# Optimization experiments

Measured on AMD Instinct MI355X. Metric: run time of the kernel, lower is better.

Reference implementation:

```python
import jax, jax.numpy as jnp
import numpy as np

EPS_NORM = 1e-7   # Normalize module eps (added to norm)
EPS_COS = 1e-8    # torch F.cosine_similarity default eps (clamped denom)


def _normalize(x):
    # Normalize(power=2): x / (||x||_2 + 1e-7), norm over dim 1
    n = jnp.sqrt(jnp.sum(x * x, axis=1, keepdims=True))
    return x / (n + EPS_NORM)


def _cos_sim_matrix(f):
    # pairwise cosine similarity, matching torch cosine_similarity semantics:
    # (f_i . f_j) / max(||f_i|| * ||f_j||, eps)
    n = jnp.linalg.norm(f, axis=1)            # [N]
    denom = jnp.maximum(n[:, None] * n[None, :], EPS_COS)
    return (f @ f.T) / denom                   # [N, N]


def setup_inputs() -> dict:
    key = jax.random.key(0)
    kq, kk = jax.random.split(key)
    N, D = 4096, 1024
    feat_q = jax.random.normal(kq, (N, D), dtype=jnp.float32)
    feat_k = jax.random.normal(kk, (N, D), dtype=jnp.float32)
    return {"feat_q": feat_q, "feat_k": feat_k}


def reference(feat_q, feat_k):
    q = _normalize(feat_q)
    k = jax.lax.stop_gradient(_normalize(feat_k))  # feat_k.detach()
    Sq = _cos_sim_matrix(q)   # [N, N]
    Sk = _cos_sim_matrix(k)   # [N, N]
    N = feat_q.shape[0]
    off_diag = ~jnp.eye(N, dtype=bool)
    diff2 = (Sq - Sk) ** 2
    # mean over the N*(N-1) off-diagonal (i != j) pairs
    loss = jnp.sum(jnp.where(off_diag, diff2, 0.0)) / (N * (N - 1))
    return loss
```

## Files before the change

kernel.cpp:

```cpp
#include <hip/hip_runtime.h>
#include <hip/hip_bf16.h>
#include <stdint.h>

#define N_ROWS 4096
#define DIMS   1024
#define BM 128
#define BN 128
#define BK 64
#define TGRID 32
#define NTILES 528

typedef __attribute__((ext_vector_type(8))) short short8;
typedef __attribute__((ext_vector_type(4))) float f32x4;

__device__ __forceinline__ unsigned short f2bf(float f) {
  union { float f; unsigned int u; } c; c.f = f;
  unsigned int u = c.u;
  unsigned int r = (u + 0x7fffu + ((u >> 16) & 1u)) >> 16;
  return (unsigned short)r;
}

__device__ __forceinline__ void async_cp16(const unsigned short* g, void* lds) {
  __builtin_amdgcn_global_load_lds(
      (const __attribute__((address_space(1))) void*)g,
      (__attribute__((address_space(3))) void*)lds, 16, 0, 0);
}

__global__ __launch_bounds__(256) void normalize_bf16_kernel(
    const float* __restrict__ fq, const float* __restrict__ fk,
    unsigned short* __restrict__ qn, unsigned short* __restrict__ kn,
    float* __restrict__ out) {
  if (blockIdx.x == 0 && blockIdx.y == 0 && threadIdx.x == 0) out[0] = 0.0f;
  const int w = threadIdx.x >> 6;
  const int lane = threadIdx.x & 63;
  const int row = blockIdx.x * 4 + w;
  const float* src = blockIdx.y ? fk : fq;
  unsigned short* dst = blockIdx.y ? kn : qn;
  const float4* s4 = (const float4*)(src + (size_t)row * DIMS);
  float4 v[4];
  float ss = 0.0f;
  #pragma unroll
  for (int s = 0; s < 4; ++s) {
    v[s] = s4[lane + 64 * s];
    ss += v[s].x * v[s].x + v[s].y * v[s].y + v[s].z * v[s].z + v[s].w * v[s].w;
  }
  #pragma unroll
  for (int off = 32; off > 0; off >>= 1) ss += __shfl_xor(ss, off);
  const float scale = 1.0f / sqrtf(ss);
  ushort4* d4 = (ushort4*)(dst + (size_t)row * DIMS);
  #pragma unroll
  for (int s = 0; s < 4; ++s) {
    ushort4 o;
    o.x = f2bf(v[s].x * scale);
    o.y = f2bf(v[s].y * scale);
    o.z = f2bf(v[s].z * scale);
    o.w = f2bf(v[s].w * scale);
    d4[lane + 64 * s] = o;
  }
}

__global__ __launch_bounds__(256, 2) void constloss_main_kernel(
    const unsigned short* __restrict__ qn,
    const unsigned short* __restrict__ kn,
    float* __restrict__ out) {
  __shared__ __align__(16) char smem[4 * BM * BK * 2];

  int I = 0, rem = blockIdx.x;
  while (rem >= (TGRID - I)) { rem -= (TGRID - I); ++I; }
  const int J = I + rem;

  const int tid = threadIdx.x;
  const int w = tid >> 6;
  const int lane = tid & 63;

  const unsigned short* sbase = (w & 2) ? kn : qn;
  const int rblk = (w & 1) ? J : I;
  const unsigned short* srow = sbase + (size_t)rblk * BM * DIMS;
  const int rl = lane >> 3;
  const int cl = (lane & 7) ^ rl;
  const unsigned short* gsrc0 = srow + (size_t)rl * DIMS + cl * 8;
  char* ldsTile = smem + w * (BM * BK * 2);

  const int wr = w >> 1, wc = w & 1;
  const int ml = lane & 15;
  const int quad = lane >> 4;
  const int ar0 = wr * 64, bc0 = wc * 64;

  f32x4 accq[4][4] = {};
  f32x4 acck[4][4] = {};

  for (int kk = 0; kk < DIMS; kk += BK) {
    const unsigned short* g = gsrc0 + kk;
    #pragma unroll
    for (int s = 0; s < 16; ++s)
      async_cp16(g + s * 8 * DIMS, ldsTile + s * 1024);
    __syncthreads();

    #pragma unroll
    for (int ks = 0; ks < BK; ks += 32) {
      const int slot = (((ks >> 3) | quad) ^ (ml & 7)) * 16;
      short8 aq[4], bq[4], ak[4], bk[4];
      #pragma unroll
      for (int i = 0; i < 4; ++i) {
        const int ra = (ar0 + i * 16 + ml) * (BK * 2);
        const int rb = (bc0 + i * 16 + ml) * (BK * 2);
        aq[i] = *(const short8*)(smem + 0     + ra + slot);
        bq[i] = *(const short8*)(smem + 16384 + rb + slot);
        ak[i] = *(const short8*)(smem + 32768 + ra + slot);
        bk[i] = *(const short8*)(smem + 49152 + rb + slot);
      }
      #pragma unroll
      for (int i = 0; i < 4; ++i) {
        #pragma unroll
        for (int j = 0; j < 4; ++j) {
          accq[i][j] = __builtin_amdgcn_mfma_f32_16x16x32_bf16(aq[i], bq[j], accq[i][j], 0, 0, 0);
          acck[i][j] = __builtin_amdgcn_mfma_f32_16x16x32_bf16(ak[i], bk[j], acck[i][j], 0, 0, 0);
        }
      }
    }
    __syncthreads();
  }

  float local = 0.0f;
  #pragma unroll
  for (int i = 0; i < 4; ++i) {
    #pragma unroll
    for (int j = 0; j < 4; ++j) {
      #pragma unroll
      for (int p = 0; p < 4; ++p) {
        const float d = accq[i][j][p] - acck[i][j][p];
        float t = d * d;
        if (I == J) {
          const int gr = ar0 + i * 16 + quad * 4 + p;
          const int gc = bc0 + j * 16 + ml;
          if (gr == gc) t = 0.0f;
        }
        local += t;
      }
    }
  }
  if (I != J) local *= 2.0f;

  #pragma unroll
  for (int off = 32; off > 0; off >>= 1) local += __shfl_xor(local, off);
  __syncthreads();
  if (lane == 0) ((float*)smem)[w] = local;
  __syncthreads();
  if (tid == 0) {
    const float t = ((float*)smem)[0] + ((float*)smem)[1] +
                    ((float*)smem)[2] + ((float*)smem)[3];
    atomicAdd(out, t * (1.0f / 16773120.0f));
  }
}

extern "C" void kernel_launch(void* const* d_in, const int* in_sizes, int n_in,
                              void* d_out, int out_size, void* d_ws, size_t ws_size,
                              hipStream_t stream) {
  const float* fq = (const float*)d_in[0];
  const float* fk = (const float*)d_in[1];
  unsigned short* qn = (unsigned short*)d_ws;
  unsigned short* kn = qn + (size_t)N_ROWS * DIMS;
  float* out = (float*)d_out;

  dim3 g1(N_ROWS / 4, 2);
  normalize_bf16_kernel<<<g1, 256, 0, stream>>>(fq, fk, qn, kn, out);
  constloss_main_kernel<<<NTILES, 256, 0, stream>>>(qn, kn, out);
}
```

Before: 132.0 us.

## Compute loss via D×D Gram of concatenated transposed features instead of N×N

The loss is reformulated so it no longer needs the two N×N similarity matrices. It uses the identity ||QQᵀ−KKᵀ||² = ||QᵀQ||² + ||KᵀK||² − 2||QᵀK||², taking the 2048×2048 Gram of the concatenated normalized features in transposed layout and applying a sign per block. New kernels compute row inverse norms, transpose and scale into bf16, and run a split-K symmetric Gram with bf16 partial slabs; a final kernel sums the slabs, squares and reduces. The aim is to halve the matmul FLOPs (D=1024 < N=4096), but it adds a transpose pass and partial-sum traffic. The diagonal exclusion is dropped, so the result is mathematically different (the diagonal term is near zero but not exactly excluded). Catastrophic cancellation in fp32/bf16 also puts accuracy at risk.

```diff
diff --git a/kernel.cpp b/kernel.cpp
--- a/kernel.cpp
+++ b/kernel.cpp
@@ -1,23 +1,27 @@
 #include <hip/hip_runtime.h>
-#include <hip/hip_bf16.h>
 #include <stdint.h>
 
 #define N_ROWS 4096
 #define DIMS   1024
 #define BM 128
-#define BN 128
 #define BK 64
-#define TGRID 32
-#define NTILES 528
+#define TG 16
+#define NTRI 136
+#define KSPLIT 4
+#define KCHUNK 1024
 
 typedef __attribute__((ext_vector_type(8))) short short8;
+typedef __attribute__((ext_vector_type(8))) unsigned short ushort8;
 typedef __attribute__((ext_vector_type(4))) float f32x4;
 
 __device__ __forceinline__ unsigned short f2bf(float f) {
   union { float f; unsigned int u; } c; c.f = f;
   unsigned int u = c.u;
-  unsigned int r = (u + 0x7fffu + ((u >> 16) & 1u)) >> 16;
-  return (unsigned short)r;
+  return (unsigned short)((u + 0x7fffu + ((u >> 16) & 1u)) >> 16);
+}
+__device__ __forceinline__ float bf2f(unsigned short v) {
+  union { float f; unsigned int u; } c; c.u = ((unsigned int)v) << 16;
+  return c.f;
 }
 
 __device__ __forceinline__ void async_cp16(const unsigned short* g, void* lds) {
@@ -26,130 +30,161 @@
       (__attribute__((address_space(3))) void*)lds, 16, 0, 0);
 }
 
-__global__ __launch_bounds__(256) void normalize_bf16_kernel(
+__global__ __launch_bounds__(256) void rownorm_kernel(
     const float* __restrict__ fq, const float* __restrict__ fk,
-    unsigned short* __restrict__ qn, unsigned short* __restrict__ kn,
-    float* __restrict__ out) {
+    float* __restrict__ invq, float* __restrict__ invk, float* __restrict__ out) {
   if (blockIdx.x == 0 && blockIdx.y == 0 && threadIdx.x == 0) out[0] = 0.0f;
-  const int w = threadIdx.x >> 6;
-  const int lane = threadIdx.x & 63;
+  const int w = threadIdx.x >> 6, lane = threadIdx.x & 63;
   const int row = blockIdx.x * 4 + w;
   const float* src = blockIdx.y ? fk : fq;
-  unsigned short* dst = blockIdx.y ? kn : qn;
+  float* dst = blockIdx.y ? invk : invq;
   const float4* s4 = (const float4*)(src + (size_t)row * DIMS);
-  float4 v[4];
   float ss = 0.0f;
   #pragma unroll
   for (int s = 0; s < 4; ++s) {
-    v[s] = s4[lane + 64 * s];
-    ss += v[s].x * v[s].x + v[s].y * v[s].y + v[s].z * v[s].z + v[s].w * v[s].w;
+    float4 v = s4[lane + 64 * s];
+    ss += v.x * v.x + v.y * v.y + v.z * v.z + v.w * v.w;
   }
   #pragma unroll
   for (int off = 32; off > 0; off >>= 1) ss += __shfl_xor(ss, off);
-  const float scale = 1.0f / sqrtf(ss);
-  ushort4* d4 = (ushort4*)(dst + (size_t)row * DIMS);
-  #pragma unroll
-  for (int s = 0; s < 4; ++s) {
-    ushort4 o;
-    o.x = f2bf(v[s].x * scale);
-    o.y = f2bf(v[s].y * scale);
-    o.z = f2bf(v[s].z * scale);
-    o.w = f2bf(v[s].w * scale);
-    d4[lane + 64 * s] = o;
-  }
-}
-
-__global__ __launch_bounds__(256, 2) void constloss_main_kernel(
-    const unsigned short* __restrict__ qn,
-    const unsigned short* __restrict__ kn,
-    float* __restrict__ out) {
-  __shared__ __align__(16) char smem[4 * BM * BK * 2];
-
-  int I = 0, rem = blockIdx.x;
-  while (rem >= (TGRID - I)) { rem -= (TGRID - I); ++I; }
+  if (lane == 0) dst[row] = 1.0f / sqrtf(ss);
+}
+
+__global__ __launch_bounds__(256) void transpose_scale_kernel(
+    const float* __restrict__ fq, const float* __restrict__ fk,
+    const float* __restrict__ invq, const float* __restrict__ invk,
+    unsigned short* __restrict__ Mt) {
+  __shared__ unsigned short tile[64][260];
+  const int i0 = blockIdx.x * 256;
+  const int a0 = blockIdx.y * 64;
+  const int w = threadIdx.x >> 6, lane = threadIdx.x & 63;
+  const float* src;
+  const float* inv;
+  int acol;
+  if (a0 < DIMS) { src = fq; inv = invq; acol = a0 + lane; }
+  else           { src = fk; inv = invk; acol = a0 - DIMS + lane; }
+
+  for (int c0 = 0; c0 < 64; c0 += 4) {
+    ushort4 v;
+    unsigned short* vp = (unsigned short*)&v;
+    #pragma unroll
+    for (int c = 0; c < 4; ++c) {
+      const int i = i0 + w * 64 + c0 + c;
+      vp[c] = f2bf(src[(size_t)i * DIMS + acol] * inv[i]);
+    }
+    *(ushort4*)&tile[lane][w * 64 + c0] = v;
+  }
+  __syncthreads();
+  #pragma unroll
+  for (int r = 0; r < 16; ++r) {
+    const int al = w * 16 + r;
+    ushort4 v = *(const ushort4*)&tile[al][lane * 4];
+    *(ushort4*)(Mt + (size_t)(a0 + al) * N_ROWS + i0 + lane * 4) = v;
+  }
+}
+
+__global__ __launch_bounds__(256, 4) void gram_partial_kernel(
+    const unsigned short* __restrict__ Mt, unsigned short* __restrict__ Gp) {
+  __shared__ __align__(16) char smem[2 * BM * BK * 2];
+
+  const int t = blockIdx.x >> 2;
+  const int kc = blockIdx.x & 3;
+  int I = 0, rem = t;
+  while (rem >= (TG - I)) { rem -= (TG - I); ++I; }
   const int J = I + rem;
 
-  const int tid = threadIdx.x;
-  const int w = tid >> 6;
-  const int lane = tid & 63;
-
-  const unsigned short* sbase = (w & 2) ? kn : qn;
-  const int rblk = (w & 1) ? J : I;
-  const unsigned short* srow = sbase + (size_t)rblk * BM * DIMS;
+  const int tid = threadIdx.x, w = tid >> 6, lane = tid & 63;
+
+  const int isB = w >> 1;
+  const int rblk = isB ? J : I;
   const int rl = lane >> 3;
   const int cl = (lane & 7) ^ rl;
-  const unsigned short* gsrc0 = srow + (size_t)rl * DIMS + cl * 8;
-  char* ldsTile = smem + w * (BM * BK * 2);
+  const bool skipStage = (isB && I == J);
+  const unsigned short* gsrc0 =
+      Mt + (size_t)(rblk * BM + (w & 1) * 64 + rl) * N_ROWS + kc * KCHUNK + cl * 8;
+  char* ldsBase = smem + isB * 16384 + (w & 1) * 8192;
+  const int bOff = (I == J) ? 0 : 16384;
 
   const int wr = w >> 1, wc = w & 1;
-  const int ml = lane & 15;
-  const int quad = lane >> 4;
+  const int ml = lane & 15, quad = lane >> 4;
   const int ar0 = wr * 64, bc0 = wc * 64;
 
-  f32x4 accq[4][4] = {};
-  f32x4 acck[4][4] = {};
-
-  for (int kk = 0; kk < DIMS; kk += BK) {
-    const unsigned short* g = gsrc0 + kk;
-    #pragma unroll
-    for (int s = 0; s < 16; ++s)
-      async_cp16(g + s * 8 * DIMS, ldsTile + s * 1024);
+  f32x4 acc[4][4] = {};
+
+  for (int kk = 0; kk < KCHUNK; kk += BK) {
+    if (!skipStage) {
+      const unsigned short* g = gsrc0 + kk;
+      #pragma unroll
+      for (int s = 0; s < 8; ++s)
+        async_cp16(g + (size_t)s * 8 * N_ROWS, ldsBase + s * 1024);
+    }
     __syncthreads();
-
     #pragma unroll
     for (int ks = 0; ks < BK; ks += 32) {
       const int slot = (((ks >> 3) | quad) ^ (ml & 7)) * 16;
-      short8 aq[4], bq[4], ak[4], bk[4];
+      short8 a[4], b[4];
       #pragma unroll
       for (int i = 0; i < 4; ++i) {
         const int ra = (ar0 + i * 16 + ml) * (BK * 2);
         const int rb = (bc0 + i * 16 + ml) * (BK * 2);
-        aq[i] = *(const short8*)(smem + 0     + ra + slot);
-        bq[i] = *(const short8*)(smem + 16384 + rb + slot);
-        ak[i] = *(const short8*)(smem + 32768 + ra + slot);
-        bk[i] = *(const short8*)(smem + 49152 + rb + slot);
+        a[i] = *(const short8*)(smem + ra + slot);
+        b[i] = *(const short8*)(smem + bOff + rb + slot);
       }
       #pragma unroll
-      for (int i = 0; i < 4; ++i) {
+      for (int i = 0; i < 4; ++i)
         #pragma unroll
-        for (int j = 0; j < 4; ++j) {
-          accq[i][j] = __builtin_amdgcn_mfma_f32_16x16x32_bf16(aq[i], bq[j], accq[i][j], 0, 0, 0);
-          acck[i][j] = __builtin_amdgcn_mfma_f32_16x16x32_bf16(ak[i], bk[j], acck[i][j], 0, 0, 0);
-        }
-      }
+        for (int j = 0; j < 4; ++j)
+          acc[i][j] = __builtin_amdgcn_mfma_f32_16x16x32_bf16(a[i], b[j], acc[i][j], 0, 0, 0);
     }
     __syncthreads();
   }
 
+  unsigned short* slab = Gp + (size_t)blockIdx.x * (BM * BM);
+  #pragma unroll
+  for (int i = 0; i < 4; ++i)
+    #pragma unroll
+    for (int j = 0; j < 4; ++j)
+      #pragma unroll
+      for (int p = 0; p < 4; ++p) {
+        const int r = ar0 + i * 16 + quad * 4 + p;
+        const int c = bc0 + j * 16 + ml;
+        slab[r * BM + c] = f2bf(acc[i][j][p]);
+      }
+}
+
+__global__ __launch_bounds__(256) void square_reduce_kernel(
+    const unsigned short* __restrict__ Gp, float* __restrict__ out) {
+  __shared__ float wsum[4];
+  const int t = blockIdx.x >> 3;
+  const int seg = blockIdx.x & 7;
+  int I = 0, rem = t;
+  while (rem >= (TG - I)) { rem -= (TG - I); ++I; }
+  const int J = I + rem;
+
+  const unsigned short* base =
+      Gp + (size_t)t * (KSPLIT * BM * BM) + seg * 2048 + threadIdx.x * 8;
+  float s[8] = {0, 0, 0, 0, 0, 0, 0, 0};
+  #pragma unroll
+  for (int kc = 0; kc < KSPLIT; ++kc) {
+    const ushort8 v = *(const ushort8*)(base + kc * (BM * BM));
+    #pragma unroll
+    for (int x = 0; x < 8; ++x) s[x] += bf2f(v[x]);
+  }
   float local = 0.0f;
   #pragma unroll
-  for (int i = 0; i < 4; ++i) {
-    #pragma unroll
-    for (int j = 0; j < 4; ++j) {
-      #pragma unroll
-      for (int p = 0; p < 4; ++p) {
-        const float d = accq[i][j][p] - acck[i][j][p];
-        float t = d * d;
-        if (I == J) {
-          const int gr = ar0 + i * 16 + quad * 4 + p;
-          const int gc = bc0 + j * 16 + ml;
-          if (gr == gc) t = 0.0f;
-        }
-        local += t;
-      }
-    }
-  }
-  if (I != J) local *= 2.0f;
+  for (int x = 0; x < 8; ++x) local += s[x] * s[x];
+
+  const float sgn = ((I < 8) == (J < 8)) ? 1.0f : -1.0f;
+  local *= (I == J ? 1.0f : 2.0f) * sgn;
 
   #pragma unroll
   for (int off = 32; off > 0; off >>= 1) local += __shfl_xor(local, off);
+  const int w = threadIdx.x >> 6, lane = threadIdx.x & 63;
+  if (lane == 0) wsum[w] = local;
   __syncthreads();
-  if (lane == 0) ((float*)smem)[w] = local;
-  __syncthreads();
-  if (tid == 0) {
-    const float t = ((float*)smem)[0] + ((float*)smem)[1] +
-                    ((float*)smem)[2] + ((float*)smem)[3];
-    atomicAdd(out, t * (1.0f / 16773120.0f));
+  if (threadIdx.x == 0) {
+    const float ts = wsum[0] + wsum[1] + wsum[2] + wsum[3];
+    atomicAdd(out, ts * (1.0f / 16773120.0f));
   }
 }
 
@@ -158,11 +193,14 @@
                               hipStream_t stream) {
   const float* fq = (const float*)d_in[0];
   const float* fk = (const float*)d_in[1];
-  unsigned short* qn = (unsigned short*)d_ws;
-  unsigned short* kn = qn + (size_t)N_ROWS * DIMS;
+  float* invq = (float*)d_ws;
+  float* invk = invq + N_ROWS;
+  unsigned short* Mt = (unsigned short*)((char*)d_ws + 32768);
+  unsigned short* Gp = Mt + (size_t)2048 * N_ROWS;
   float* out = (float*)d_out;
 
-  dim3 g1(N_ROWS / 4, 2);
-  normalize_bf16_kernel<<<g1, 256, 0, stream>>>(fq, fk, qn, kn, out);
-  constloss_main_kernel<<<NTILES, 256, 0, stream>>>(qn, kn, out);
-}
+  rownorm_kernel<<<dim3(N_ROWS / 4, 2), 256, 0, stream>>>(fq, fk, invq, invk, out);
+  transpose_scale_kernel<<<dim3(16, 32), 256, 0, stream>>>(fq, fk, invq, invk, Mt);
+  gram_partial_kernel<<<NTRI * KSPLIT, 256, 0, stream>>>(Mt, Gp);
+  square_reduce_kernel<<<NTRI * 8, 256, 0, stream>>>(Gp, out);
+}
```

Measured after the change: 120.7 us. 1.09x faster.
